# Performance work log

Measured on AMD Instinct MI355X. Metric: run time of the kernel, lower is better.

## Reference

```python
import jax, jax.numpy as jnp
import numpy as np

N, M, D = 131072, 32, 32


def setup_inputs() -> dict:
    key = jax.random.key(0)
    k1, k2, k3, k4 = jax.random.split(key, 4)
    # scale points/centers so Mahalanobis distances are O(1) and exp(-d) is well-conditioned
    points = 0.2 * jax.random.normal(k1, (N, D), dtype=jnp.float32)
    centers = 0.2 * jax.random.normal(k2, (M, D), dtype=jnp.float32)
    covs_inv_sqrt = jnp.eye(D, dtype=jnp.float32)[None] + 0.05 * jax.random.normal(k3, (M, D, D), dtype=jnp.float32)
    weights = jax.random.normal(k4, (M,), dtype=jnp.float32)
    return {"points": points, "centers": centers, "covs_inv_sqrt": covs_inv_sqrt, "weights": weights}


def reference(points, centers, covs_inv_sqrt, weights):
    # refresh(): covs_inv = L @ L^T, coefs = softmax(weights) * sqrt(det(covs_inv))
    A = jnp.einsum('mdk,mek->mde', covs_inv_sqrt, covs_inv_sqrt)  # (M, D, D)
    coefs = jax.nn.softmax(weights) * jnp.sqrt(jnp.linalg.det(A))  # (M,)

    # weightedsqdist: d_nm = (x_n - c_m)^T A_m (x_n - c_m), expanded to avoid (N,M,D) diff
    xAx = jnp.einsum('nd,mde,ne->nm', points, A, points)          # (N, M)
    Ac = jnp.einsum('mde,me->md', A, centers)                     # (M, D)
    xAc = jnp.einsum('nd,md->nm', points, Ac)                     # (N, M)
    cAc = jnp.einsum('md,md->m', centers, Ac)                     # (M,)
    dists = xAx - 2.0 * xAc + cAc[None, :]

    # coefs * exp(-dists) with mixture reduction over centers (KeOps sum over j)
    return jnp.exp(-dists) @ coefs  # (N,)
```

## Files before the change

kernel.cpp:

```cpp
#include <hip/hip_runtime.h>
#include <hip/hip_bf16.h>


#define D 32
#define M 32
#define WT 2

typedef __attribute__((ext_vector_type(8))) short short8;
typedef __attribute__((ext_vector_type(4))) float f32x4;

__device__ __forceinline__ unsigned short f2bf_rne(float f) {
  unsigned int u = __float_as_uint(f);
  return (unsigned short)((u + 0x7FFFu + ((u >> 16) & 1u)) >> 16);
}

#define DPP_ADD(x, ctrl) \
  ((x) + __int_as_float(__builtin_amdgcn_mov_dpp(__float_as_int(x), (ctrl), 0xf, 0xf, true)))

#define SCL 1.2011224087864498f

__global__ __launch_bounds__(64) void gmm_pre(
    const float* __restrict__ centers, const float* __restrict__ L,
    const float* __restrict__ weights,
    float2* __restrict__ CNp, float* __restrict__ LC,
    unsigned short* __restrict__ LH, unsigned short* __restrict__ LL) {
  __shared__ float U[D][D + 1];
  __shared__ float C2s[D];
  const int m = blockIdx.x;
  const int t = threadIdx.x;
  const float* Lm = L + m * (D * D);

  if (t < D) {
    for (int k = 0; k < D; ++k) U[t][k] = Lm[t * D + k];
    float acc = 0.f;
    for (int d = 0; d < D; ++d) acc = fmaf(centers[m * D + d], Lm[d * D + t], acc);
    C2s[t] = acc;
  }

  {
    const int col = t & 15;
    const int dbase = 8 * (t >> 4);
    for (int kt = 0; kt < 2; ++kt) {
      for (int j = 0; j < 8; ++j) {
        const int d = dbase + j;
        const int k = kt * 16 + col;
        float v = Lm[d * D + k] * SCL;
        unsigned int hi = __float_as_uint(v) & 0xFFFF0000u;
        float lo = v - __uint_as_float(hi);
        size_t off = (((size_t)(m * 2 + kt)) * 64 + t) * 8 + j;
        LH[off] = (unsigned short)(hi >> 16);
        LL[off] = f2bf_rne(lo);
      }
    }
  }
  __syncthreads();

  if (t < 16) CNp[m * 16 + t] = make_float2(-SCL * C2s[t], -SCL * C2s[16 + t]);

  for (int p = 0; p < D - 1; ++p) {
    if (t > p && t < D) {
      float f = U[t][p] / U[p][p];
      for (int k = p; k < D; ++k) U[t][k] -= f * U[p][k];
    }
    __syncthreads();
  }
  if (t == 0) {
    float det = 1.f;
    for (int i = 0; i < D; ++i) det *= U[i][i];
    float mx = -1e30f;
    for (int j = 0; j < M; ++j) mx = fmaxf(mx, weights[j]);
    float s = 0.f;
    for (int j = 0; j < M; ++j) s += __expf(weights[j] - mx);
    float coef = (__expf(weights[m] - mx) / s) * fabsf(det);
    LC[m] = log2f(coef);
  }
}

__global__ __launch_bounds__(1024, 4) void gmm_main(
    const float* __restrict__ points,
    const float2* __restrict__ CNp, const float* __restrict__ LC,
    const unsigned short* __restrict__ LH, const unsigned short* __restrict__ LL,
    float* __restrict__ out, int N) {
  __shared__ unsigned short sLH[M * 2 * 64 * 8];
  __shared__ unsigned short sLL[M * 2 * 64 * 8];
  __shared__ float2 sCN[M * 16];

  const int tid = threadIdx.x;
  const int lane = tid & 63;
  const int wave = tid >> 6;
  const int col = lane & 15;
  const int g = lane >> 4;

  {
    const uint4* src = reinterpret_cast<const uint4*>(LH);
    uint4* dst = reinterpret_cast<uint4*>(sLH);
#pragma unroll
    for (int i = 0; i < 4; ++i) dst[tid + i * 1024] = src[tid + i * 1024];
    src = reinterpret_cast<const uint4*>(LL);
    dst = reinterpret_cast<uint4*>(sLL);
#pragma unroll
    for (int i = 0; i < 4; ++i) dst[tid + i * 1024] = src[tid + i * 1024];
    if (tid < M * 16) sCN[tid] = CNp[tid];
  }

  const int tileBase = (blockIdx.x * 16 + wave) * (WT * 16);

  const bool b0 = (lane >> 2) & 1;
  const bool b1 = (lane >> 2) & 2;

  short8 xh[WT], xl[WT];
#pragma unroll
  for (int t = 0; t < WT; ++t) {
    const float* p = points + (size_t)(tileBase + t * 16 + col) * D + 8 * g;
    float4 a = *reinterpret_cast<const float4*>(p);
    float4 b = *reinterpret_cast<const float4*>(p + 4);
    float v[8] = {a.x, a.y, a.z, a.w, b.x, b.y, b.z, b.w};
    unsigned int hiu[8];
    unsigned int lou[8];
#pragma unroll
    for (int j = 0; j < 8; ++j) {
      unsigned int u = __float_as_uint(v[j]);
      hiu[j] = u & 0xFFFF0000u;
      lou[j] = __float_as_uint(v[j] - __uint_as_float(hiu[j]));
    }
    union { short8 s; unsigned int w[4]; } H, Lo;
#pragma unroll
    for (int jj = 0; jj < 4; ++jj) {
      H.w[jj]  = __builtin_amdgcn_perm(hiu[2 * jj + 1], hiu[2 * jj], 0x07060302);
      Lo.w[jj] = __builtin_amdgcn_perm(lou[2 * jj + 1], lou[2 * jj], 0x07060302);
    }
    xh[t] = H.s;
    xl[t] = Lo.s;
  }

  __syncthreads();

  float result[WT];
#pragma unroll
  for (int t = 0; t < WT; ++t) result[t] = 0.f;

  const short8* bh_base = reinterpret_cast<const short8*>(sLH);
  const short8* bl_base = reinterpret_cast<const short8*>(sLL);

#pragma unroll 2
  for (int m = 0; m < M; ++m) {
    short8 bh0 = bh_base[(m * 2 + 0) * 64 + lane];
    short8 bh1 = bh_base[(m * 2 + 1) * 64 + lane];
    short8 bl0 = bl_base[(m * 2 + 0) * 64 + lane];
    short8 bl1 = bl_base[(m * 2 + 1) * 64 + lane];
    const float2 cn = sCN[m * 16 + col];
    const float lc = LC[m];

#pragma unroll
    for (int t = 0; t < WT; ++t) {
      f32x4 acc0 = (f32x4){cn.x, cn.x, cn.x, cn.x};
      f32x4 acc1 = (f32x4){cn.y, cn.y, cn.y, cn.y};
      acc0 = __builtin_amdgcn_mfma_f32_16x16x32_bf16(xh[t], bh0, acc0, 0, 0, 0);
      acc0 = __builtin_amdgcn_mfma_f32_16x16x32_bf16(xl[t], bh0, acc0, 0, 0, 0);
      acc0 = __builtin_amdgcn_mfma_f32_16x16x32_bf16(xh[t], bl0, acc0, 0, 0, 0);
      acc1 = __builtin_amdgcn_mfma_f32_16x16x32_bf16(xh[t], bh1, acc1, 0, 0, 0);
      acc1 = __builtin_amdgcn_mfma_f32_16x16x32_bf16(xl[t], bh1, acc1, 0, 0, 0);
      acc1 = __builtin_amdgcn_mfma_f32_16x16x32_bf16(xh[t], bl1, acc1, 0, 0, 0);

      float s0 = fmaf(acc0[0], acc0[0], acc1[0] * acc1[0]);
      float s1 = fmaf(acc0[1], acc0[1], acc1[1] * acc1[1]);
      float s2 = fmaf(acc0[2], acc0[2], acc1[2] * acc1[2]);
      float s3 = fmaf(acc0[3], acc0[3], acc1[3] * acc1[3]);
      s0 = DPP_ADD(s0, 0x128); s0 = DPP_ADD(s0, 0x124);
      s1 = DPP_ADD(s1, 0x128); s1 = DPP_ADD(s1, 0x124);
      s2 = DPP_ADD(s2, 0x128); s2 = DPP_ADD(s2, 0x124);
      s3 = DPP_ADD(s3, 0x128); s3 = DPP_ADD(s3, 0x124);
      float v = b1 ? (b0 ? s3 : s2) : (b0 ? s1 : s0);
      v = DPP_ADD(v, 0xB1);
      v = DPP_ADD(v, 0x4E);
      result[t] += exp2f(lc - v);
    }
  }

  if ((lane & 3) == 0) {
    const int q = (lane >> 2) & 3;
#pragma unroll
    for (int t = 0; t < WT; ++t)
      out[tileBase + t * 16 + 4 * g + q] = result[t];
  }
}

extern "C" void kernel_launch(void* const* d_in, const int* in_sizes, int n_in,
                              void* d_out, int out_size, void* d_ws, size_t ws_size,
                              hipStream_t stream) {
  const float* points  = (const float*)d_in[0];
  const float* centers = (const float*)d_in[1];
  const float* L       = (const float*)d_in[2];
  const float* weights = (const float*)d_in[3];
  float* out = (float*)d_out;
  const int N = in_sizes[0] / D;

  char* ws = (char*)d_ws;
  float2* CNp         = (float2*)ws;
  float* LC           = (float*)(ws + 4096);
  unsigned short* LHf = (unsigned short*)(ws + 8192);
  unsigned short* LLf = (unsigned short*)(ws + 8192 + 65536);

  gmm_pre<<<M, 64, 0, stream>>>(centers, L, weights, CNp, LC, LHf, LLf);

  gmm_main<<<N / (16 * WT * 16), 1024, 0, stream>>>(
      points, CNp, LC, LHf, LLf, out, N);
}
```

Baseline: 119.8 us.

## Split mixture components across blocks with partial sums and separate reduce kernel

```diff
diff --git a/kernel.cpp b/kernel.cpp
--- a/kernel.cpp
+++ b/kernel.cpp
@@ -4,7 +4,9 @@
 
 #define D 32
 #define M 32
-#define WT 2
+#define WT 4
+#define GROUPS 4
+#define MPG 8
 
 typedef __attribute__((ext_vector_type(8))) short short8;
 typedef __attribute__((ext_vector_type(4))) float f32x4;
@@ -76,34 +78,21 @@
   }
 }
 
-__global__ __launch_bounds__(1024, 4) void gmm_main(
+__global__ __launch_bounds__(256, 4) void gmm_main(
     const float* __restrict__ points,
     const float2* __restrict__ CNp, const float* __restrict__ LC,
     const unsigned short* __restrict__ LH, const unsigned short* __restrict__ LL,
-    float* __restrict__ out, int N) {
-  __shared__ unsigned short sLH[M * 2 * 64 * 8];
-  __shared__ unsigned short sLL[M * 2 * 64 * 8];
-  __shared__ float2 sCN[M * 16];
-
-  const int tid = threadIdx.x;
-  const int lane = tid & 63;
-  const int wave = tid >> 6;
+    float* __restrict__ parts, int N) {
+  const int pblocks = N >> 8;
+  const int group = blockIdx.x / pblocks;
+  const int pblk = blockIdx.x - group * pblocks;
+  const int m0 = group * MPG;
+
+  const int lane = threadIdx.x & 63;
+  const int wave = threadIdx.x >> 6;
   const int col = lane & 15;
   const int g = lane >> 4;
-
-  {
-    const uint4* src = reinterpret_cast<const uint4*>(LH);
-    uint4* dst = reinterpret_cast<uint4*>(sLH);
-#pragma unroll
-    for (int i = 0; i < 4; ++i) dst[tid + i * 1024] = src[tid + i * 1024];
-    src = reinterpret_cast<const uint4*>(LL);
-    dst = reinterpret_cast<uint4*>(sLL);
-#pragma unroll
-    for (int i = 0; i < 4; ++i) dst[tid + i * 1024] = src[tid + i * 1024];
-    if (tid < M * 16) sCN[tid] = CNp[tid];
-  }
-
-  const int tileBase = (blockIdx.x * 16 + wave) * (WT * 16);
+  const int tileBase = (pblk * 4 + wave) * (WT * 16);
 
   const bool b0 = (lane >> 2) & 1;
   const bool b1 = (lane >> 2) & 2;
@@ -133,22 +122,21 @@
     xl[t] = Lo.s;
   }
 
-  __syncthreads();
-
   float result[WT];
 #pragma unroll
   for (int t = 0; t < WT; ++t) result[t] = 0.f;
 
-  const short8* bh_base = reinterpret_cast<const short8*>(sLH);
-  const short8* bl_base = reinterpret_cast<const short8*>(sLL);
+  const short8* bh_base = reinterpret_cast<const short8*>(LH);
+  const short8* bl_base = reinterpret_cast<const short8*>(LL);
 
 #pragma unroll 2
-  for (int m = 0; m < M; ++m) {
+  for (int mi = 0; mi < MPG; ++mi) {
+    const int m = m0 + mi;
     short8 bh0 = bh_base[(m * 2 + 0) * 64 + lane];
     short8 bh1 = bh_base[(m * 2 + 1) * 64 + lane];
     short8 bl0 = bl_base[(m * 2 + 0) * 64 + lane];
     short8 bl1 = bl_base[(m * 2 + 1) * 64 + lane];
-    const float2 cn = sCN[m * 16 + col];
+    const float2 cn = CNp[m * 16 + col];
     const float lc = LC[m];
 
 #pragma unroll
@@ -179,9 +167,20 @@
 
   if ((lane & 3) == 0) {
     const int q = (lane >> 2) & 3;
+    float* dst = parts + (size_t)group * N + tileBase;
 #pragma unroll
     for (int t = 0; t < WT; ++t)
-      out[tileBase + t * 16 + 4 * g + q] = result[t];
+      dst[t * 16 + 4 * g + q] = result[t];
+  }
+}
+
+__global__ __launch_bounds__(256) void gmm_reduce(
+    const float* __restrict__ parts, float* __restrict__ out, int N) {
+  const int n = blockIdx.x * 256 + threadIdx.x;
+  if (n < N) {
+    float s = (parts[n] + parts[(size_t)N + n]) +
+              (parts[2 * (size_t)N + n] + parts[3 * (size_t)N + n]);
+    out[n] = s;
   }
 }
 
@@ -200,9 +199,13 @@
   float* LC           = (float*)(ws + 4096);
   unsigned short* LHf = (unsigned short*)(ws + 8192);
   unsigned short* LLf = (unsigned short*)(ws + 8192 + 65536);
+  float* parts        = (float*)(ws + 262144);
 
   gmm_pre<<<M, 64, 0, stream>>>(centers, L, weights, CNp, LC, LHf, LLf);
 
-  gmm_main<<<N / (16 * WT * 16), 1024, 0, stream>>>(
-      points, CNp, LC, LHf, LLf, out, N);
-}
+  const int pblocks = N >> 8;
+  gmm_main<<<GROUPS * pblocks, 256, 0, stream>>>(
+      points, CNp, LC, LHf, LLf, parts, N);
+
+  gmm_reduce<<<(N + 255) / 256, 256, 0, stream>>>(parts, out, N);
+}
```

After: 143.8 us. 1.2x slower.
